# Kernel tuning notes

Hardware: AMD Instinct MI355X
Metric: run time of the kernel (lower is better)

Reference implementation:

```python
import jax, jax.numpy as jnp
import numpy as np

N_NODES = 50000   # r_mat is [N_NODES, N_NODES] sparse
N_REL = 1000      # number of relations (rows of dual_layer)
D = 128           # node / relation feature dim
NNZ = 800000      # number of edges (nnz of r_mat)


def setup_inputs() -> dict:
    key = jax.random.key(0)
    k1, k2, k3, k4, k5, k6 = jax.random.split(key, 6)
    return {
        "inlayer": jax.random.normal(k1, (N_NODES, D), jnp.float32),
        "dual_layer": jax.random.normal(k2, (N_REL, D), jnp.float32),
        # Conv1d(in=D, out=1, kernel=1): weight [1, D, 1] -> vector [D], bias [1]
        "conv_w": jax.random.normal(k3, (D,), jnp.float32) * (1.0 / np.sqrt(D)),
        "conv_b": jax.random.normal(k4, (1,), jnp.float32) * 0.01,
        # COO indices of r_mat: row = destination node, col = source node
        "edge_idx": jax.random.randint(k5, (2, NNZ), 0, N_NODES, dtype=jnp.int32),
        # r_mat._values(): integer relation id per edge
        "edge_rel": jax.random.randint(k6, (NNZ,), 0, N_REL, dtype=jnp.int32),
    }


def reference(inlayer, dual_layer, conv_w, conv_b, edge_idx, edge_rel):
    # conv1d with kernel_size=1 over [1, D, n_rel] == per-relation linear -> [n_rel]
    scores = dual_layer @ conv_w + conv_b[0]
    # gather per-edge logit by relation id
    logits = scores[edge_rel]                                  # [nnz]
    # NOTE: original applies leaky_relu then softmax GLOBALLY over all nnz edges
    coefs = jax.nn.softmax(jax.nn.leaky_relu(logits))          # [nnz]
    row, col = edge_idx[0], edge_idx[1]
    # sparse-dense matmul: out[r] = sum_{e: row[e]=r} coefs[e] * inlayer[col[e]]
    out = jax.ops.segment_sum(coefs[:, None] * inlayer[col], row,
                              num_segments=N_NODES)            # [N, D]
    # act_func=None path of the original forward
    return out
```

## Files before the change

### kernel.cpp

```cpp
#include <hip/hip_runtime.h>
#include <hip/hip_fp16.h>
#include <math.h>

#define N_NODES 50000
#define N_REL   1000
#define D       128
#define NNZ     800000

#define RB    512
#define NBIN  98
#define CAP   10240
#define CH    1024
#define NCH   ((NNZ + CH - 1) / CH)
#define K1T   256
#define K1E   (CH / K1T)
#define SRB   64
#define CAPL  1536

__global__ void __launch_bounds__(K1T)
k1_kernel(const int* __restrict__ rows, const int* __restrict__ cols,
          const int* __restrict__ rel, const float* __restrict__ dual,
          const float* __restrict__ conv_w, const float* __restrict__ conv_b,
          const float* __restrict__ inlayer, float* __restrict__ exp_scores,
          unsigned* __restrict__ relcnt, unsigned* __restrict__ bincur,
          unsigned long long* __restrict__ binbuf, __half2* __restrict__ hinl) {
    __shared__ unsigned long long sbuf[CH];
    __shared__ unsigned char sbin[CH];
    __shared__ unsigned lcnt[NBIN], lstart[NBIN], lgb[NBIN];
    __shared__ unsigned lrel[N_REL];
    __shared__ unsigned w0sum;
    int t = threadIdx.x;
    int gtid = blockIdx.x * K1T + t;
    int lane = t & 63;

    int wid = gtid >> 6;
    if (wid < N_REL) {
        const float* row = dual + (long)wid * D;
        float s = row[lane] * conv_w[lane] + row[lane + 64] * conv_w[lane + 64];
        #pragma unroll
        for (int off = 32; off > 0; off >>= 1) s += __shfl_down(s, off);
        if (lane == 0) {
            float v = s + conv_b[0];
            v = (v >= 0.f) ? v : 0.01f * v;
            exp_scores[wid] = expf(v);
        }
    }

    const float4* src4 = (const float4*)inlayer;
    uint2* dst2 = (uint2*)hinl;
    for (int i = gtid; i < N_NODES * D / 4; i += NCH * K1T) {
        float4 f = src4[i];
        __half2 h0 = __floats2half2_rn(f.x, f.y);
        __half2 h1 = __floats2half2_rn(f.z, f.w);
        uint2 o; o.x = *(unsigned*)&h0; o.y = *(unsigned*)&h1;
        dst2[i] = o;
    }

    if (t < NBIN) lcnt[t] = 0;
    for (int i = t; i < N_REL; i += K1T) lrel[i] = 0;
    __syncthreads();

    int n = NNZ - blockIdx.x * CH; if (n > CH) n = CH;
    int base4 = blockIdx.x * (CH / 4);

    int       ebin[K1E];
    unsigned  erank[K1E];
    unsigned long long epack[K1E];
    bool has = (4 * t < n);
    int4 rr, cc, qq;
    if (has) {
        rr = ((const int4*)rows)[base4 + t];
        cc = ((const int4*)cols)[base4 + t];
        qq = ((const int4*)rel)[base4 + t];
    }
    #pragma unroll
    for (int k = 0; k < K1E; ++k) {
        if (has) {
            int r = (k == 0) ? rr.x : (k == 1) ? rr.y : (k == 2) ? rr.z : rr.w;
            int c = (k == 0) ? cc.x : (k == 1) ? cc.y : (k == 2) ? cc.z : cc.w;
            int q = (k == 0) ? qq.x : (k == 1) ? qq.y : (k == 2) ? qq.z : qq.w;
            int b = r >> 9;
            epack[k] = (unsigned long long)(unsigned)c
                     | ((unsigned long long)(unsigned)q << 16)
                     | ((unsigned long long)(unsigned)(r & 511) << 26);
            ebin[k] = b;
            erank[k] = atomicAdd(&lcnt[b], 1u);
            atomicAdd(&lrel[q], 1u);
        } else ebin[k] = -1;
    }
    __syncthreads();

    unsigned v = (t < NBIN) ? lcnt[t] : 0u;
    if (t < 128) {
        #pragma unroll
        for (int off = 1; off < 64; off <<= 1) {
            unsigned y = __shfl_up(v, off);
            if (lane >= off) v += y;
        }
        if (t == 63) w0sum = v;
    }
    __syncthreads();
    if (t >= 64 && t < 128) v += w0sum;
    if (t < NBIN) {
        lstart[t] = v - lcnt[t];
        lgb[t] = atomicAdd(&bincur[t * 16], lcnt[t]);
    }
    for (int i = t; i < N_REL; i += K1T) {
        unsigned cv = lrel[i];
        if (cv) atomicAdd(&relcnt[i], cv);
    }
    __syncthreads();

    #pragma unroll
    for (int k = 0; k < K1E; ++k) {
        if (ebin[k] >= 0) {
            unsigned p = lstart[ebin[k]] + erank[k];
            sbuf[p] = epack[k];
            sbin[p] = (unsigned char)ebin[k];
        }
    }
    __syncthreads();

    #pragma unroll
    for (int k = 0; k < K1E; ++k) {
        int j = k * K1T + t;
        if (j < n) {
            int b = sbin[j];
            unsigned slot = lgb[b] + (unsigned)j - lstart[b];
            if (slot < CAP)
                binbuf[(unsigned long long)b * CAP + slot] = sbuf[j];
        }
    }
}

__global__ void __launch_bounds__(512)
k2_kernel(const unsigned* __restrict__ bincur,
          const unsigned long long* __restrict__ binbuf,
          const float* __restrict__ exp_scores,
          const unsigned* __restrict__ relcnt,
          const __half2* __restrict__ hinl, float* __restrict__ out) {
    __shared__ unsigned ulist[CAPL];
    __shared__ unsigned list[CAPL];
    __shared__ unsigned cnt[SRB], ex[SRB], cur[SRB];
    __shared__ unsigned total;
    int t = threadIdx.x, lane = t & 63, w = t >> 6;
    int b   = blockIdx.x >> 3;
    int sub = blockIdx.x & 7;

    if (t < SRB) cnt[t] = 0;
    if (t == 0) total = 0;

    float dsum = 0.f;
    for (int i = lane; i < N_REL; i += 64)
        dsum += (float)relcnt[i] * exp_scores[i];
    #pragma unroll
    for (int off = 32; off > 0; off >>= 1) dsum += __shfl_down(dsum, off);
    float inv = 1.0f / __shfl(dsum, 0);

    __syncthreads();

    unsigned nb = bincur[b * 16]; if (nb > CAP) nb = CAP;
    const unsigned long long* bb = binbuf + (unsigned long long)b * CAP;

    for (unsigned e = t; e < nb; e += 512u) {
        unsigned long long pk = bb[e];
        unsigned u = (unsigned)(pk >> 26) & 511u;
        if ((u >> 6) == (unsigned)sub) {
            unsigned lo = (unsigned)pk;
            unsigned idx = atomicAdd(&total, 1u);
            if (idx < CAPL) ulist[idx] = lo;
            atomicAdd(&cnt[lo >> 26], 1u);
        }
    }
    __syncthreads();

    if (t < 64) {
        unsigned c0 = cnt[t];
        unsigned v = c0;
        #pragma unroll
        for (int off = 1; off < 64; off <<= 1) {
            unsigned y = __shfl_up(v, off);
            if (lane >= off) v += y;
        }
        ex[t] = v - c0;
        cur[t] = v - c0;
    }
    __syncthreads();

    unsigned tot = total; if (tot > CAPL) tot = CAPL;
    for (unsigned i = t; i < tot; i += 512u) {
        unsigned lo = ulist[i];
        unsigned idx = atomicAdd(&cur[lo >> 26], 1u);
        if (idx < CAPL) list[idx] = lo & 0x3FFFFFFu;
    }
    __syncthreads();

    int quad = lane >> 4;
    int l16  = lane & 15;
    for (int i = 0; i < 8; ++i) {
        int rl = w * 8 + i;
        int node = b * RB + sub * SRB + rl;
        int s0 = (int)ex[rl];
        int e0 = s0 + (int)cnt[rl];
        if (e0 > CAPL) e0 = CAPL;
        float a0=0.f,a1=0.f,a2=0.f,a3=0.f,a4=0.f,a5=0.f,a6=0.f,a7=0.f;
        for (int base = s0; base < e0; base += 64) {
            int rem = e0 - base; if (rem > 64) rem = 64;
            int px = 0, py = 0;
            if (lane < rem) {
                unsigned pk = list[base + lane];
                px = (int)(pk & 0xFFFFu);
                py = __float_as_int(exp_scores[pk >> 16]);
            }
            for (int jj = 0; jj < rem; jj += 16) {
                #pragma unroll
                for (int k = 0; k < 16; k += 4) {
                    if (jj + k < rem) {
                        int idx = jj + k + quad;
                        int   c = __shfl(px, idx);
                        float wv = __int_as_float(__shfl(py, idx));
                        const __half2* hp = hinl + (long)c * (D / 2) + l16 * 4;
                        uint4 hv = *(const uint4*)hp;
                        float2 f0 = __half22float2(*(const __half2*)&hv.x);
                        float2 f1 = __half22float2(*(const __half2*)&hv.y);
                        float2 f2 = __half22float2(*(const __half2*)&hv.z);
                        float2 f3 = __half22float2(*(const __half2*)&hv.w);
                        a0 += wv * f0.x; a1 += wv * f0.y;
                        a2 += wv * f1.x; a3 += wv * f1.y;
                        a4 += wv * f2.x; a5 += wv * f2.y;
                        a6 += wv * f3.x; a7 += wv * f3.y;
                    }
                }
            }
        }
        #define COMB(x) x += __shfl(x, lane ^ 16); x += __shfl(x, lane ^ 32);
        COMB(a0) COMB(a1) COMB(a2) COMB(a3) COMB(a4) COMB(a5) COMB(a6) COMB(a7)
        #undef COMB
        if (lane < 32 && node < N_NODES) {
            float4 o;
            int hi = (lane >> 4) & 1;
            if (hi) { o.x = a4*inv; o.y = a5*inv; o.z = a6*inv; o.w = a7*inv; }
            else    { o.x = a0*inv; o.y = a1*inv; o.z = a2*inv; o.w = a3*inv; }
            *(float4*)(out + (long)node * D + l16 * 8 + hi * 4) = o;
        }
    }
}

extern "C" void kernel_launch(void* const* d_in, const int* in_sizes, int n_in,
                              void* d_out, int out_size, void* d_ws, size_t ws_size,
                              hipStream_t stream) {
    const float* inlayer  = (const float*)d_in[0];
    const float* dual     = (const float*)d_in[1];
    const float* conv_w   = (const float*)d_in[2];
    const float* conv_b   = (const float*)d_in[3];
    const int*   edge_idx = (const int*)d_in[4];
    const int*   edge_rel = (const int*)d_in[5];
    float* out = (float*)d_out;
    const int* rows = edge_idx;
    const int* cols = edge_idx + NNZ;

    char* ws = (char*)d_ws;
    float*              exp_scores = (float*)             (ws);
    unsigned*           relcnt     = (unsigned*)          (ws + 4096);
    unsigned*           bincur     = (unsigned*)          (ws + 8192);
    unsigned long long* binbuf     = (unsigned long long*)(ws + 16384);
    __half2*            hinl       = (__half2*)           (ws + 16384 + 8028160);

    hipMemsetAsync(ws + 4096, 0, 12288, stream);

    k1_kernel<<<NCH, K1T, 0, stream>>>(rows, cols, edge_rel, dual, conv_w, conv_b,
                                       inlayer, exp_scores, relcnt, bincur,
                                       binbuf, hinl);
    k2_kernel<<<NBIN * 8, 512, 0, stream>>>(bincur, binbuf, exp_scores, relcnt,
                                            hinl, out);
}
```

Measured before the change: 153.5 us.

## Split score kernel out, accumulate softmax denominator in binning pass, unroll bin scan

Moves the per-relation score and exp computation into a separate small kernel launched first. The binning kernel then sums exp_scores per edge directly into a global float denominator, replacing the shared per-relation histogram and its global atomics. This also removes the 1000-element reduction that every k2 block repeated. The binning kernel's chunk and block size are doubled, and k2's bin scan issues four loads before processing them. The cost is an extra kernel launch, a float atomic whose summation order is not fixed, and k1 now reading exp_scores it previously did not need.

```diff
diff --git a/kernel.cpp b/kernel.cpp
--- a/kernel.cpp
+++ b/kernel.cpp
@@ -10,41 +10,44 @@
 #define RB    512
 #define NBIN  98
 #define CAP   10240
-#define CH    1024
+#define CH    2048
 #define NCH   ((NNZ + CH - 1) / CH)
-#define K1T   256
+#define K1T   512
 #define K1E   (CH / K1T)
 #define SRB   64
 #define CAPL  1536
 
+__global__ void __launch_bounds__(512)
+k0_kernel(const float* __restrict__ dual, const float* __restrict__ conv_w,
+          const float* __restrict__ conv_b, float* __restrict__ exp_scores) {
+    int wid = (blockIdx.x * 512 + threadIdx.x) >> 6;
+    int lane = threadIdx.x & 63;
+    if (wid >= N_REL) return;
+    const float* row = dual + (long)wid * D;
+    float s = row[lane] * conv_w[lane] + row[lane + 64] * conv_w[lane + 64];
+    #pragma unroll
+    for (int off = 32; off > 0; off >>= 1) s += __shfl_down(s, off);
+    if (lane == 0) {
+        float v = s + conv_b[0];
+        v = (v >= 0.f) ? v : 0.01f * v;
+        exp_scores[wid] = expf(v);
+    }
+}
+
 __global__ void __launch_bounds__(K1T)
 k1_kernel(const int* __restrict__ rows, const int* __restrict__ cols,
-          const int* __restrict__ rel, const float* __restrict__ dual,
-          const float* __restrict__ conv_w, const float* __restrict__ conv_b,
-          const float* __restrict__ inlayer, float* __restrict__ exp_scores,
-          unsigned* __restrict__ relcnt, unsigned* __restrict__ bincur,
-          unsigned long long* __restrict__ binbuf, __half2* __restrict__ hinl) {
+          const int* __restrict__ rel, const float* __restrict__ inlayer,
+          const float* __restrict__ exp_scores, float* __restrict__ denom,
+          unsigned* __restrict__ bincur, unsigned long long* __restrict__ binbuf,
+          __half2* __restrict__ hinl) {
     __shared__ unsigned long long sbuf[CH];
     __shared__ unsigned char sbin[CH];
     __shared__ unsigned lcnt[NBIN], lstart[NBIN], lgb[NBIN];
-    __shared__ unsigned lrel[N_REL];
+    __shared__ float fpart[8];
     __shared__ unsigned w0sum;
     int t = threadIdx.x;
     int gtid = blockIdx.x * K1T + t;
-    int lane = t & 63;
-
-    int wid = gtid >> 6;
-    if (wid < N_REL) {
-        const float* row = dual + (long)wid * D;
-        float s = row[lane] * conv_w[lane] + row[lane + 64] * conv_w[lane + 64];
-        #pragma unroll
-        for (int off = 32; off > 0; off >>= 1) s += __shfl_down(s, off);
-        if (lane == 0) {
-            float v = s + conv_b[0];
-            v = (v >= 0.f) ? v : 0.01f * v;
-            exp_scores[wid] = expf(v);
-        }
-    }
+    int lane = t & 63, w = t >> 6;
 
     const float4* src4 = (const float4*)inlayer;
     uint2* dst2 = (uint2*)hinl;
@@ -57,7 +60,6 @@
     }
 
     if (t < NBIN) lcnt[t] = 0;
-    for (int i = t; i < N_REL; i += K1T) lrel[i] = 0;
     __syncthreads();
 
     int n = NNZ - blockIdx.x * CH; if (n > CH) n = CH;
@@ -66,6 +68,7 @@
     int       ebin[K1E];
     unsigned  erank[K1E];
     unsigned long long epack[K1E];
+    float dsum = 0.f;
     bool has = (4 * t < n);
     int4 rr, cc, qq;
     if (has) {
@@ -85,9 +88,12 @@
                      | ((unsigned long long)(unsigned)(r & 511) << 26);
             ebin[k] = b;
             erank[k] = atomicAdd(&lcnt[b], 1u);
-            atomicAdd(&lrel[q], 1u);
+            dsum += exp_scores[q];
         } else ebin[k] = -1;
     }
+    #pragma unroll
+    for (int off = 32; off > 0; off >>= 1) dsum += __shfl_down(dsum, off);
+    if (lane == 0) fpart[w] = dsum;
     __syncthreads();
 
     unsigned v = (t < NBIN) ? lcnt[t] : 0u;
@@ -99,15 +105,17 @@
         }
         if (t == 63) w0sum = v;
     }
+    if (t == 0) {
+        float s = 0.f;
+        #pragma unroll
+        for (int k = 0; k < 8; ++k) s += fpart[k];
+        atomicAdd(denom, s);
+    }
     __syncthreads();
     if (t >= 64 && t < 128) v += w0sum;
     if (t < NBIN) {
         lstart[t] = v - lcnt[t];
         lgb[t] = atomicAdd(&bincur[t * 16], lcnt[t]);
-    }
-    for (int i = t; i < N_REL; i += K1T) {
-        unsigned cv = lrel[i];
-        if (cv) atomicAdd(&relcnt[i], cv);
     }
     __syncthreads();
 
@@ -137,7 +145,7 @@
 k2_kernel(const unsigned* __restrict__ bincur,
           const unsigned long long* __restrict__ binbuf,
           const float* __restrict__ exp_scores,
-          const unsigned* __restrict__ relcnt,
+          const float* __restrict__ denom,
           const __half2* __restrict__ hinl, float* __restrict__ out) {
     __shared__ unsigned ulist[CAPL];
     __shared__ unsigned list[CAPL];
@@ -149,28 +157,34 @@
 
     if (t < SRB) cnt[t] = 0;
     if (t == 0) total = 0;
-
-    float dsum = 0.f;
-    for (int i = lane; i < N_REL; i += 64)
-        dsum += (float)relcnt[i] * exp_scores[i];
-    #pragma unroll
-    for (int off = 32; off > 0; off >>= 1) dsum += __shfl_down(dsum, off);
-    float inv = 1.0f / __shfl(dsum, 0);
+    float inv = 1.0f / *denom;
 
     __syncthreads();
 
     unsigned nb = bincur[b * 16]; if (nb > CAP) nb = CAP;
     const unsigned long long* bb = binbuf + (unsigned long long)b * CAP;
 
-    for (unsigned e = t; e < nb; e += 512u) {
-        unsigned long long pk = bb[e];
-        unsigned u = (unsigned)(pk >> 26) & 511u;
-        if ((u >> 6) == (unsigned)sub) {
-            unsigned lo = (unsigned)pk;
-            unsigned idx = atomicAdd(&total, 1u);
-            if (idx < CAPL) ulist[idx] = lo;
-            atomicAdd(&cnt[lo >> 26], 1u);
-        }
+    for (unsigned e0 = 0; e0 < nb; e0 += 2048u) {
+        unsigned i0 = e0 + (unsigned)t;
+        unsigned long long p0 = 0, p1 = 0, p2 = 0, p3 = 0;
+        bool g0 = i0 < nb, g1 = i0 + 512u < nb,
+             g2 = i0 + 1024u < nb, g3 = i0 + 1536u < nb;
+        if (g0) p0 = bb[i0];
+        if (g1) p1 = bb[i0 + 512u];
+        if (g2) p2 = bb[i0 + 1024u];
+        if (g3) p3 = bb[i0 + 1536u];
+        #define PROC(pk, g)                                                  \
+        if (g) {                                                             \
+            unsigned u_ = (unsigned)((pk) >> 26) & 511u;                     \
+            if ((u_ >> 6) == (unsigned)sub) {                                \
+                unsigned lo_ = (unsigned)(pk);                               \
+                unsigned idx_ = atomicAdd(&total, 1u);                       \
+                if (idx_ < CAPL) ulist[idx_] = lo_;                          \
+                atomicAdd(&cnt[lo_ >> 26], 1u);                              \
+            }                                                                \
+        }
+        PROC(p0, g0) PROC(p1, g1) PROC(p2, g2) PROC(p3, g3)
+        #undef PROC
     }
     __syncthreads();
 
@@ -261,16 +275,16 @@
 
     char* ws = (char*)d_ws;
     float*              exp_scores = (float*)             (ws);
-    unsigned*           relcnt     = (unsigned*)          (ws + 4096);
+    float*              denom      = (float*)             (ws + 4096);
     unsigned*           bincur     = (unsigned*)          (ws + 8192);
     unsigned long long* binbuf     = (unsigned long long*)(ws + 16384);
     __half2*            hinl       = (__half2*)           (ws + 16384 + 8028160);
 
     hipMemsetAsync(ws + 4096, 0, 12288, stream);
 
-    k1_kernel<<<NCH, K1T, 0, stream>>>(rows, cols, edge_rel, dual, conv_w, conv_b,
-                                       inlayer, exp_scores, relcnt, bincur,
-                                       binbuf, hinl);
-    k2_kernel<<<NBIN * 8, 512, 0, stream>>>(bincur, binbuf, exp_scores, relcnt,
+    k0_kernel<<<125, 512, 0, stream>>>(dual, conv_w, conv_b, exp_scores);
+    k1_kernel<<<NCH, K1T, 0, stream>>>(rows, cols, edge_rel, inlayer, exp_scores,
+                                       denom, bincur, binbuf, hinl);
+    k2_kernel<<<NBIN * 8, 512, 0, stream>>>(bincur, binbuf, exp_scores, denom,
                                             hinl, out);
 }
```

Result: faster. 139.9 us (-8.9%).
